# Performance work log

Hardware: AMD Instinct MI355X
Metric: run time of the kernel (lower is better)

The kernel has to match this reference:

```python
import jax, jax.numpy as jnp
import numpy as np

EPS = 1e-5
MAX_NORM = 1.0 - 1e-5  # clamp for atanh / ball projection


def mob_add(u, v):
    # Mobius addition on each d_ball (last dim), c=1
    uv = jnp.sum(u * v, axis=-1, keepdims=True)
    uu = jnp.sum(u * u, axis=-1, keepdims=True)
    vv = jnp.sum(v * v, axis=-1, keepdims=True)
    num = (1.0 + 2.0 * uv + vv) * u + (1.0 - uu) * v
    den = 1.0 + 2.0 * uv + uu * vv
    return num / jnp.maximum(den, EPS)


def log_map_zero(y):
    # log map at origin, per ball (last dim)
    n = jnp.linalg.norm(y, axis=-1, keepdims=True)
    n_c = jnp.clip(n, EPS, MAX_NORM)
    return jnp.arctanh(n_c) * y / n_c


def mob_mat_mul_d(W, x, d):
    # W: (n_in, d, n_out, d); x: (B, n_in, d) -> (B, n_out, d)
    # Mobius matvec on the flattened product-ball representation.
    B = x.shape[0]
    x_f = x.reshape(B, -1)                      # (B, n_in*d)
    W_f = W.reshape(x_f.shape[-1], -1)          # (n_in*d, n_out*d)
    Mx = x_f @ W_f                              # (B, n_out*d)
    x_n = jnp.clip(jnp.linalg.norm(x_f, axis=-1, keepdims=True), EPS, MAX_NORM)
    Mx_n = jnp.maximum(jnp.linalg.norm(Mx, axis=-1, keepdims=True), EPS)
    res = jnp.tanh(Mx_n / x_n * jnp.arctanh(x_n)) * (Mx / Mx_n)
    return res.reshape(B, -1, d)


def mob_pointwise_prod(x, u):
    # diagonal Mobius scaling of hyperbolic x by euclidean gate u, per ball
    ux = u * x
    x_n = jnp.clip(jnp.linalg.norm(x, axis=-1, keepdims=True), EPS, MAX_NORM)
    ux_n = jnp.maximum(jnp.linalg.norm(ux, axis=-1, keepdims=True), EPS)
    return jnp.tanh(ux_n / x_n * jnp.arctanh(x_n)) * (ux / ux_n)


def transition(W, h, U, x, b, d):
    Wh = mob_mat_mul_d(W, h, d)
    Ux = mob_mat_mul_d(U, x, d)
    return mob_add(mob_add(Wh, Ux), b)


def setup_inputs() -> dict:
    key = jax.random.key(0)
    ks = jax.random.split(key, 8)
    B, I, H, D = 16384, 256, 256, 4
    k = (1.0 / H) ** 0.5
    # scale points to lie strictly inside the Poincare ball
    hyp_x = 0.02 * jax.random.normal(ks[0], (B, I, D), dtype=jnp.float32)
    hidden = 0.02 * jax.random.normal(ks[1], (B, H, D), dtype=jnp.float32)
    mk = lambda kk, n_in: jax.random.uniform(kk, (n_in, D, H, D), minval=-k, maxval=k, dtype=jnp.float32)
    return dict(
        hyp_x=hyp_x, hidden=hidden,
        w_z=mk(ks[2], H), w_r=mk(ks[3], H), w_h=mk(ks[4], H),
        u_z=mk(ks[5], I), u_r=mk(ks[6], I), u_h=mk(ks[7], I),
        b_z=jnp.zeros((H, D), jnp.float32),
        b_r=jnp.zeros((H, D), jnp.float32),
        b_h=jnp.zeros((H, D), jnp.float32),
    )


def reference(hyp_x, hidden, w_z, w_r, w_h, u_z, u_r, u_h, b_z, b_r, b_h):
    d = hyp_x.shape[-1]
    z = jax.nn.sigmoid(log_map_zero(transition(w_z, hidden, u_z, hyp_x, b_z, d)))
    r = jax.nn.sigmoid(log_map_zero(transition(w_r, hidden, u_r, hyp_x, b_r, d)))
    r_point_h = mob_pointwise_prod(hidden, r)
    # NOTE: original code uses u_r here (not u_h) -- kept faithful
    h_tilde = transition(w_h, r_point_h, u_r, hyp_x, b_h, d)
    minus_h_oplus_htilde = mob_add(-hidden, h_tilde)
    new_h = mob_add(hidden, mob_pointwise_prod(minus_h_oplus_htilde, z))
    return new_h
```

## Files before the change

### kernel.cpp

```cpp
#include <hip/hip_runtime.h>
#include <stdint.h>

#define EPSF 1e-5f
#define MAXNF (1.0f - 1e-5f)

typedef __attribute__((ext_vector_type(8))) short short8;
typedef __attribute__((ext_vector_type(4))) float floatx4;

__device__ __forceinline__ unsigned short f2bf(float f){
  union { float f; uint32_t u; } v; v.f = f;
  return (unsigned short)((v.u + 0x7FFFu + ((v.u >> 16) & 1u)) >> 16);
}
__device__ __forceinline__ float bf_lo(uint32_t u){
  union { uint32_t u; float f; } v; v.u = u << 16; return v.f;
}
__device__ __forceinline__ float bf_hi(uint32_t u){
  union { uint32_t u; float f; } v; v.u = u & 0xffff0000u; return v.f;
}
__device__ __forceinline__ uint32_t cvtpk(float lo, float hi){
  uint32_t r; asm("v_cvt_pk_bf16_f32 %0, %1, %2" : "=v"(r) : "v"(lo), "v"(hi));
  return r;
}
__device__ __forceinline__ float fsqrt(float x){ return __builtin_amdgcn_sqrtf(x); }

__device__ __forceinline__ float4 ld_ball(const unsigned short* rowp, int b){
  const uint2 u = *(const uint2*)(rowp + 4*b);
  return make_float4(bf_lo(u.x), bf_hi(u.x), bf_lo(u.y), bf_hi(u.y));
}
__device__ __forceinline__ void st_ball(unsigned short* rowp, int b, float4 f){
  uint2 u; u.x = cvtpk(f.x, f.y); u.y = cvtpk(f.z, f.w);
  *(uint2*)(rowp + 4*b) = u;
}

__device__ __forceinline__ void gload16(const void* g, void* l){
  __builtin_amdgcn_global_load_lds(
      (__attribute__((address_space(1))) void*)(uintptr_t)g,
      (__attribute__((address_space(3))) void*)l, 16, 0, 0);
}

__device__ __forceinline__ float fatanh(float x){
  return 0.5f * __logf(__fdividef(1.f + x, 1.f - x));
}
__device__ __forceinline__ float ftanh_pos(float x){
  const float t = __expf(-2.f * x);
  return __fdividef(1.f - t, 1.f + t);
}
__device__ __forceinline__ float fsig(float x){
  return __fdividef(1.f, 1.f + __expf(-x));
}

__device__ __forceinline__ float wsum(float v){
  #pragma unroll
  for (int o = 32; o; o >>= 1) v += __shfl_xor(v, o);
  return v;
}

__device__ __forceinline__ float dot4(const float4 a, const float4 b){
  return a.x*b.x + a.y*b.y + a.z*b.z + a.w*b.w;
}
__device__ __forceinline__ float4 scal4(const float4 a, float s){
  return make_float4(a.x*s, a.y*s, a.z*s, a.w*s);
}
__device__ __forceinline__ float clipn(float n){ return fminf(fmaxf(n, EPSF), MAXNF); }

__device__ __forceinline__ float4 mob_add4(const float4 u, const float4 v){
  const float uv = dot4(u,v), uu = dot4(u,u), vv = dot4(v,v);
  const float cu = 1.f + 2.f*uv + vv, cv = 1.f - uu;
  const float inv = __fdividef(1.f, fmaxf(1.f + 2.f*uv + uu*vv, EPSF));
  return make_float4((cu*u.x + cv*v.x)*inv, (cu*u.y + cv*v.y)*inv,
                     (cu*u.z + cv*v.z)*inv, (cu*u.w + cv*v.w)*inv);
}
__device__ __forceinline__ float4 logmap_sig4(const float4 y){
  const float nc = clipn(fsqrt(dot4(y,y)));
  const float s = __fdividef(fatanh(nc), nc);
  return make_float4(fsig(s*y.x), fsig(s*y.y), fsig(s*y.z), fsig(s*y.w));
}
__device__ __forceinline__ float4 mob_pp4(const float4 x, const float4 u){
  const float4 ux = make_float4(u.x*x.x, u.y*x.y, u.z*x.z, u.w*x.w);
  const float xn = clipn(fsqrt(dot4(x,x)));
  const float uxn = fmaxf(fsqrt(dot4(ux,ux)), EPSF);
  const float s = __fdividef(ftanh_pos(__fdividef(uxn, xn) * fatanh(xn)), uxn);
  return scal4(ux, s);
}

__global__ void cast_norm_k(const float* __restrict__ X, unsigned short* __restrict__ Xbf,
                            float* __restrict__ nrm){
  const int lane = threadIdx.x & 63;
  const int row  = blockIdx.x*4 + (threadIdx.x >> 6);
  const float4* xr = (const float4*)(X + (size_t)row*1024);
  unsigned short* br_ = Xbf + (size_t)row*1024;
  float ss = 0.f;
  #pragma unroll
  for (int i = 0; i < 4; ++i){
    const int b = lane + 64*i;
    const float4 v = xr[b];
    st_ball(br_, b, v);
    ss += dot4(v, v);
  }
  ss = wsum(ss);
  if (lane == 0) nrm[row] = fsqrt(ss);
}

__global__ void wcast_k(const float* __restrict__ W, unsigned short* __restrict__ Wt){
  __shared__ float tile[32][33];
  const int tx = threadIdx.x, ty = threadIdx.y;
  const int k0 = blockIdx.x * 32, n0 = blockIdx.y * 32;
  #pragma unroll
  for (int i = 0; i < 4; ++i)
    tile[ty + i*8][tx] = W[(size_t)(k0 + ty + i*8) * 1024 + n0 + tx];
  __syncthreads();
  #pragma unroll
  for (int i = 0; i < 4; ++i)
    Wt[(size_t)(n0 + ty + i*8) * 1024 + k0 + tx] = f2bf(tile[tx][ty + i*8]);
}

#define NT 16

#define BARFENCE do { __builtin_amdgcn_s_barrier(); asm volatile("" ::: "memory"); } while(0)
#define LDA4(dst, MO, BUF) do { _Pragma("unroll") for (int m_=0;m_<4;++m_) \
  _Pragma("unroll") for (int k_=0;k_<2;++k_) \
    dst[m_][k_] = *(const short8*)(smem + (BUF)*32768 + abase + (MO+m_)*2048 + ((((k_<<2)+kg)^x7)<<4)); } while(0)
#define LDB2(dst, NO, BUF) do { _Pragma("unroll") for (int n_=0;n_<2;++n_) \
  _Pragma("unroll") for (int k_=0;k_<2;++k_) \
    dst[n_][k_] = *(const short8*)(smem + (BUF)*32768 + bbase + (NO+n_)*2048 + ((((k_<<2)+kg)^x7)<<4)); } while(0)
#define QUAD(AF, MO, BF, NO) do { _Pragma("unroll") for (int m_=0;m_<4;++m_) \
  _Pragma("unroll") for (int n_=0;n_<2;++n_) \
  _Pragma("unroll") for (int k_=0;k_<2;++k_) \
    acc[MO+m_][NO+n_] = __builtin_amdgcn_mfma_f32_16x16x32_bf16(AF[m_][k_], BF[n_][k_], acc[MO+m_][NO+n_], 0,0,0); } while(0)

__global__ __launch_bounds__(512, 2) void gemm8_k(const unsigned short* __restrict__ A,
                                                  const unsigned short* __restrict__ Bt,
                                                  unsigned short* __restrict__ C,
                                                  int lda, int ldc, int lnx){
  __shared__ unsigned char smem[131072];
  const int tid = threadIdx.x;
  const int lane = tid & 63, w = tid >> 6;
  const int wm = w >> 2, wn = w & 3;
  const int lr = lane & 15, kg = lane >> 4;
  const int x7 = lr & 7;

  const int wg  = blockIdx.x;
  const int xcd = wg & 7, q = wg >> 3;
  const int bx  = q & ((1 << lnx) - 1);
  const int by  = (xcd << 3) + (q >> lnx);
  const int row0 = by * 256, col0 = bx * 256;

  const int abase = (wm*128 + lr)*128;
  const int bbase = 65536 + (wn*64 + lr)*128;

  floatx4 acc[8][4] = {};

  auto stageH = [&](int regionByte, const unsigned short* src, int srow0, int ld, int kt){
    #pragma unroll
    for (int call = 0; call < 2; ++call){
      const int L  = (call << 9) + tid;
      const int rl = L >> 3;
      const int cc = (L & 7) ^ (rl & 7);
      gload16(src + (size_t)(srow0 + rl)*ld + kt*64 + cc*8,
              smem + regionByte + L*16);
    }
  };
  auto stageA = [&](int kt, int h){ stageH((kt&1)*32768 + h*16384, A, row0 + h*128, lda, kt); };
  auto stageB = [&](int kt, int h){ stageH(65536 + (kt&1)*32768 + h*16384, Bt, col0 + h*128, 1024, kt); };

  stageA(0,0); stageA(0,1); stageB(0,0); stageB(0,1);
  stageA(1,0); stageA(1,1); stageB(1,0); stageB(1,1);
  asm volatile("s_waitcnt vmcnt(8)" ::: "memory");
  BARFENCE;

  short8 aL[4][2], aH[4][2], bA[2][2], bB[2][2];
  LDA4(aL, 0, 0);
  LDB2(bA, 0, 0);

  for (int t = 0; t < NT; ++t){
    const int bufb = t & 1;
    LDB2(bB, 2, bufb);
    BARFENCE;
    __builtin_amdgcn_s_setprio(1); QUAD(aL, 0, bA, 0); __builtin_amdgcn_s_setprio(0);
    BARFENCE;
    LDA4(aH, 4, bufb);
    BARFENCE;
    __builtin_amdgcn_s_setprio(1); QUAD(aL, 0, bB, 2); __builtin_amdgcn_s_setprio(0);
    BARFENCE;
    if (t+2 < NT){
      stageB(t+2,0); stageB(t+2,1);
      asm volatile("s_waitcnt vmcnt(4)" ::: "memory");
    } else if (t+1 < NT){
      asm volatile("s_waitcnt vmcnt(0)" ::: "memory");
    }
    BARFENCE;
    __builtin_amdgcn_s_setprio(1); QUAD(aH, 4, bB, 2); __builtin_amdgcn_s_setprio(0);
    if (t+1 < NT) LDA4(aL, 0, bufb^1);
    BARFENCE;
    if (t+2 < NT){ stageA(t+2,0); stageA(t+2,1); }
    BARFENCE;
    __builtin_amdgcn_s_setprio(1); QUAD(aH, 4, bA, 0); __builtin_amdgcn_s_setprio(0);
    if (t+1 < NT) LDB2(bA, 0, bufb^1);
    BARFENCE;
  }

  const int crow = row0 + wm*128;
  const int ccol = col0 + wn*64 + lr;
  #pragma unroll
  for (int m = 0; m < 8; ++m){
    #pragma unroll
    for (int j = 0; j < 4; ++j){
      unsigned short* cp = C + (size_t)(crow + m*16 + kg*4 + j)*ldc + ccol;
      #pragma unroll
      for (int n = 0; n < 4; ++n) cp[n*16] = f2bf(acc[m][n][j]);
    }
  }
}

__global__ __launch_bounds__(256) __attribute__((amdgpu_waves_per_eu(4,4)))
void epi1_k(unsigned short* C1, unsigned short* C2, const unsigned short* hbf,
            const float* bz, const float* br,
            const float* h_nrm, const float* x_nrm, float* rph_nrm){
  const int lane = threadIdx.x & 63;
  const int row  = blockIdx.x*4 + (threadIdx.x >> 6);
  unsigned short* c1lo = C1 + (size_t)row*2048;
  unsigned short* c1hi = c1lo + 1024;
  unsigned short* c2lo = C2 + (size_t)row*2048;
  unsigned short* c2hi = c2lo + 1024;
  const unsigned short* hr = hbf + (size_t)row*1024;

  float4 mzh[4], mrh[4], mzx[4], mrx[4];
  float s0 = 0.f, s1 = 0.f, s2 = 0.f, s3 = 0.f;
  #pragma unroll
  for (int i = 0; i < 4; ++i){
    const int b = lane + 64*i;
    mzh[i] = ld_ball(c1lo, b); mrh[i] = ld_ball(c1hi, b);
    mzx[i] = ld_ball(c2lo, b); mrx[i] = ld_ball(c2hi, b);
    s0 += dot4(mzh[i], mzh[i]); s1 += dot4(mzx[i], mzx[i]);
    s2 += dot4(mrh[i], mrh[i]); s3 += dot4(mrx[i], mrx[i]);
  }
  s0 = wsum(s0); s1 = wsum(s1); s2 = wsum(s2); s3 = wsum(s3);

  const float nMzh = fmaxf(fsqrt(s0), EPSF);
  const float nMzx = fmaxf(fsqrt(s1), EPSF);
  const float nMrh = fmaxf(fsqrt(s2), EPSF);
  const float nMrx = fmaxf(fsqrt(s3), EPSF);
  const float hnc = clipn(h_nrm[row]), xnc = clipn(x_nrm[row]);
  const float atH = fatanh(hnc), atX = fatanh(xnc);
  const float swz = __fdividef(ftanh_pos(__fdividef(nMzh, hnc)*atH), nMzh);
  const float suz = __fdividef(ftanh_pos(__fdividef(nMzx, xnc)*atX), nMzx);
  const float swr = __fdividef(ftanh_pos(__fdividef(nMrh, hnc)*atH), nMrh);
  const float sur = __fdividef(ftanh_pos(__fdividef(nMrx, xnc)*atX), nMrx);

  float sr = 0.f;
  #pragma unroll
  for (int i = 0; i < 4; ++i){
    const int b = lane + 64*i;
    const float4 bz4 = ((const float4*)bz)[b];
    const float4 br4 = ((const float4*)br)[b];
    const float4 z4  = logmap_sig4(mob_add4(mob_add4(scal4(mzh[i],swz), scal4(mzx[i],suz)), bz4));
    const float4 UxR = scal4(mrx[i], sur);
    const float4 r4  = logmap_sig4(mob_add4(mob_add4(scal4(mrh[i],swr), UxR), br4));
    st_ball(c1lo, b, z4);
    st_ball(c1hi, b, UxR);
    const float4 h4  = ld_ball(hr, b);
    const float4 rph = mob_pp4(h4, r4);
    st_ball(c2lo, b, rph);
    sr += dot4(rph, rph);
  }
  sr = wsum(sr);
  if (lane == 0) rph_nrm[row] = fsqrt(sr);
}

__global__ __launch_bounds__(256) __attribute__((amdgpu_waves_per_eu(4,4)))
void epi2_k(const unsigned short* C1, const unsigned short* C2,
            const unsigned short* hbf, const float* bh,
            const float* rph_nrm, float* out){
  const int lane = threadIdx.x & 63;
  const int row  = blockIdx.x*4 + (threadIdx.x >> 6);
  const unsigned short* c1lo = C1 + (size_t)row*2048;
  const unsigned short* c1hi = c1lo + 1024;
  const unsigned short* c2hi = C2 + (size_t)row*2048 + 1024;
  const unsigned short* hr = hbf + (size_t)row*1024;
  float4* outr = (float4*)(out + (size_t)row*1024);

  float4 mh[4];
  float ss = 0.f;
  #pragma unroll
  for (int i = 0; i < 4; ++i){
    mh[i] = ld_ball(c2hi, lane + 64*i);
    ss += dot4(mh[i], mh[i]);
  }
  ss = wsum(ss);
  const float nMh = fmaxf(fsqrt(ss), EPSF);
  const float rnc = clipn(rph_nrm[row]);
  const float swh = __fdividef(ftanh_pos(__fdividef(nMh, rnc)*fatanh(rnc)), nMh);

  #pragma unroll
  for (int i = 0; i < 4; ++i){
    const int b = lane + 64*i;
    const float4 WhH = scal4(mh[i], swh);
    const float4 Ux4 = ld_ball(c1hi, b);
    const float4 bh4 = ((const float4*)bh)[b];
    const float4 ht  = mob_add4(mob_add4(WhH, Ux4), bh4);
    const float4 h4  = ld_ball(hr, b);
    const float4 nh4 = make_float4(-h4.x, -h4.y, -h4.z, -h4.w);
    const float4 m4  = mob_add4(nh4, ht);
    const float4 z4  = ld_ball(c1lo, b);
    const float4 p4  = mob_pp4(m4, z4);
    outr[b] = mob_add4(h4, p4);
  }
}

extern "C" void kernel_launch(void* const* d_in, const int* in_sizes, int n_in,
                              void* d_out, int out_size, void* d_ws, size_t ws_size,
                              hipStream_t stream) {
  (void)in_sizes; (void)n_in; (void)out_size; (void)ws_size;
  const float* hyp_x  = (const float*)d_in[0];
  const float* hidden = (const float*)d_in[1];
  const float* w_z = (const float*)d_in[2];
  const float* w_r = (const float*)d_in[3];
  const float* w_h = (const float*)d_in[4];
  const float* u_z = (const float*)d_in[5];
  const float* u_r = (const float*)d_in[6];
  const float* b_z = (const float*)d_in[8];
  const float* b_r = (const float*)d_in[9];
  const float* b_h = (const float*)d_in[10];
  float* out = (float*)d_out;

  const size_t NROW = 16384, MAT = NROW*1024;
  unsigned short* hbf = (unsigned short*)d_ws;
  unsigned short* xbf = hbf + MAT;
  unsigned short* C1  = xbf + MAT;
  unsigned short* wzr = C1 + 2*MAT;
  unsigned short* uzr = wzr + 2*1048576;
  unsigned short* wht = uzr + 2*1048576;
  float* h_n   = (float*)(wht + 1048576);
  float* x_n   = h_n + NROW;
  float* rph_n = x_n + NROW;
  unsigned short* C2 = (unsigned short*)d_out;

  cast_norm_k<<<dim3(4096), dim3(256), 0, stream>>>(hidden, hbf, h_n);
  cast_norm_k<<<dim3(4096), dim3(256), 0, stream>>>(hyp_x, xbf, x_n);

  dim3 wg(32, 32), wb(32, 8);
  wcast_k<<<wg, wb, 0, stream>>>(w_z, wzr);
  wcast_k<<<wg, wb, 0, stream>>>(w_r, wzr + 1048576);
  wcast_k<<<wg, wb, 0, stream>>>(u_z, uzr);
  wcast_k<<<wg, wb, 0, stream>>>(u_r, uzr + 1048576);
  wcast_k<<<wg, wb, 0, stream>>>(w_h, wht);

  gemm8_k<<<dim3(512), dim3(512), 0, stream>>>(hbf, wzr, C1, 1024, 2048, 3);
  gemm8_k<<<dim3(512), dim3(512), 0, stream>>>(xbf, uzr, C2, 1024, 2048, 3);

  epi1_k<<<dim3(4096), dim3(256), 0, stream>>>(C1, C2, hbf, b_z, b_r, h_n, x_n, rph_n);

  gemm8_k<<<dim3(256), dim3(512), 0, stream>>>(C2, wht, C2 + 1024, 2048, 2048, 2);

  epi2_k<<<dim3(4096), dim3(256), 0, stream>>>(C1, C2, hbf, b_h, rph_n, out);
}
```

Before: 324.0 us.

## Switch GEMM to 32x32x16 MFMA tiles and merge cast kernel launches

The GEMM inner loop now issues 32x32x16 bf16 MFMAs instead of 16x16x32 ones. The shared-memory fragment loads, accumulator layout and epilogue store mapping are rewritten to match the larger tile shape. This is meant to cut the number of MFMA and LDS instructions for the same work. Separately, the two activation cast kernels and the five weight cast/transpose kernels are each merged into a single launch to reduce launch overhead. The new swizzle and row mapping add risk of LDS bank conflicts or indexing errors.

```diff
diff --git a/kernel.cpp b/kernel.cpp
--- a/kernel.cpp
+++ b/kernel.cpp
@@ -6,6 +6,7 @@
 
 typedef __attribute__((ext_vector_type(8))) short short8;
 typedef __attribute__((ext_vector_type(4))) float floatx4;
+typedef __attribute__((ext_vector_type(16))) float floatx16;
 
 __device__ __forceinline__ unsigned short f2bf(float f){
   union { float f; uint32_t u; } v; v.f = f;
@@ -83,12 +84,17 @@
   return scal4(ux, s);
 }
 
-__global__ void cast_norm_k(const float* __restrict__ X, unsigned short* __restrict__ Xbf,
-                            float* __restrict__ nrm){
+__global__ void cast2_k(const float* __restrict__ H, const float* __restrict__ X,
+                        unsigned short* __restrict__ Hbf, unsigned short* __restrict__ Xbf,
+                        float* __restrict__ h_n, float* __restrict__ x_n){
+  int blk = blockIdx.x;
+  const float* src; unsigned short* dst; float* nrm;
+  if (blk < 4096){ src = H; dst = Hbf; nrm = h_n; }
+  else { src = X; dst = Xbf; nrm = x_n; blk -= 4096; }
   const int lane = threadIdx.x & 63;
-  const int row  = blockIdx.x*4 + (threadIdx.x >> 6);
-  const float4* xr = (const float4*)(X + (size_t)row*1024);
-  unsigned short* br_ = Xbf + (size_t)row*1024;
+  const int row  = blk*4 + (threadIdx.x >> 6);
+  const float4* xr = (const float4*)(src + (size_t)row*1024);
+  unsigned short* br_ = dst + (size_t)row*1024;
   float ss = 0.f;
   #pragma unroll
   for (int i = 0; i < 4; ++i){
@@ -101,7 +107,20 @@
   if (lane == 0) nrm[row] = fsqrt(ss);
 }
 
-__global__ void wcast_k(const float* __restrict__ W, unsigned short* __restrict__ Wt){
+__global__ void wcast5_k(const float* __restrict__ w_z, const float* __restrict__ w_r,
+                         const float* __restrict__ u_z, const float* __restrict__ u_r,
+                         const float* __restrict__ w_h,
+                         unsigned short* __restrict__ wzr, unsigned short* __restrict__ uzr,
+                         unsigned short* __restrict__ wht){
+  const int m = blockIdx.z;
+  const float* W; unsigned short* Wt;
+  switch (m){
+    case 0: W = w_z; Wt = wzr;           break;
+    case 1: W = w_r; Wt = wzr + 1048576; break;
+    case 2: W = u_z; Wt = uzr;           break;
+    case 3: W = u_r; Wt = uzr + 1048576; break;
+    default: W = w_h; Wt = wht;          break;
+  }
   __shared__ float tile[32][33];
   const int tx = threadIdx.x, ty = threadIdx.y;
   const int k0 = blockIdx.x * 32, n0 = blockIdx.y * 32;
@@ -117,16 +136,14 @@
 #define NT 16
 
 #define BARFENCE do { __builtin_amdgcn_s_barrier(); asm volatile("" ::: "memory"); } while(0)
-#define LDA4(dst, MO, BUF) do { _Pragma("unroll") for (int m_=0;m_<4;++m_) \
-  _Pragma("unroll") for (int k_=0;k_<2;++k_) \
-    dst[m_][k_] = *(const short8*)(smem + (BUF)*32768 + abase + (MO+m_)*2048 + ((((k_<<2)+kg)^x7)<<4)); } while(0)
-#define LDB2(dst, NO, BUF) do { _Pragma("unroll") for (int n_=0;n_<2;++n_) \
-  _Pragma("unroll") for (int k_=0;k_<2;++k_) \
-    dst[n_][k_] = *(const short8*)(smem + (BUF)*32768 + bbase + (NO+n_)*2048 + ((((k_<<2)+kg)^x7)<<4)); } while(0)
-#define QUAD(AF, MO, BF, NO) do { _Pragma("unroll") for (int m_=0;m_<4;++m_) \
-  _Pragma("unroll") for (int n_=0;n_<2;++n_) \
-  _Pragma("unroll") for (int k_=0;k_<2;++k_) \
-    acc[MO+m_][NO+n_] = __builtin_amdgcn_mfma_f32_16x16x32_bf16(AF[m_][k_], BF[n_][k_], acc[MO+m_][NO+n_], 0,0,0); } while(0)
+#define LDA8(dst, MT0, BUF) do { _Pragma("unroll") for (int mt_=0;mt_<2;++mt_) \
+  _Pragma("unroll") for (int ks_=0;ks_<4;++ks_) \
+    dst[mt_][ks_] = *(const short8*)(smem + (BUF)*32768 + abase + (MT0+mt_)*4096 + ((((ks_<<1)+hi)^x7)<<4)); } while(0)
+#define LDB4(dst, NT0, BUF) do { _Pragma("unroll") for (int ks_=0;ks_<4;++ks_) \
+    dst[ks_] = *(const short8*)(smem + (BUF)*32768 + bbase + (NT0)*4096 + ((((ks_<<1)+hi)^x7)<<4)); } while(0)
+#define OCT(AF, MO, BF, NO) do { _Pragma("unroll") for (int mt_=0;mt_<2;++mt_) \
+  _Pragma("unroll") for (int ks_=0;ks_<4;++ks_) \
+    acc[MO+mt_][NO] = __builtin_amdgcn_mfma_f32_32x32x16_bf16(AF[mt_][ks_], BF[ks_], acc[MO+mt_][NO], 0,0,0); } while(0)
 
 __global__ __launch_bounds__(512, 2) void gemm8_k(const unsigned short* __restrict__ A,
                                                   const unsigned short* __restrict__ Bt,
@@ -136,8 +153,8 @@
   const int tid = threadIdx.x;
   const int lane = tid & 63, w = tid >> 6;
   const int wm = w >> 2, wn = w & 3;
-  const int lr = lane & 15, kg = lane >> 4;
-  const int x7 = lr & 7;
+  const int l31 = lane & 31, hi = lane >> 5;
+  const int x7 = lane & 7;
 
   const int wg  = blockIdx.x;
   const int xcd = wg & 7, q = wg >> 3;
@@ -145,10 +162,10 @@
   const int by  = (xcd << 3) + (q >> lnx);
   const int row0 = by * 256, col0 = bx * 256;
 
-  const int abase = (wm*128 + lr)*128;
-  const int bbase = 65536 + (wn*64 + lr)*128;
-
-  floatx4 acc[8][4] = {};
+  const int abase = (wm*128 + l31)*128;
+  const int bbase = 65536 + (wn*64 + l31)*128;
+
+  floatx16 acc[4][2] = {};
 
   auto stageH = [&](int regionByte, const unsigned short* src, int srow0, int ld, int kt){
     #pragma unroll
@@ -168,19 +185,19 @@
   asm volatile("s_waitcnt vmcnt(8)" ::: "memory");
   BARFENCE;
 
-  short8 aL[4][2], aH[4][2], bA[2][2], bB[2][2];
-  LDA4(aL, 0, 0);
-  LDB2(bA, 0, 0);
+  short8 aLo[2][4], aHi[2][4], bA[4], bB[4];
+  LDA8(aLo, 0, 0);
+  LDB4(bA, 0, 0);
 
   for (int t = 0; t < NT; ++t){
     const int bufb = t & 1;
-    LDB2(bB, 2, bufb);
-    BARFENCE;
-    __builtin_amdgcn_s_setprio(1); QUAD(aL, 0, bA, 0); __builtin_amdgcn_s_setprio(0);
-    BARFENCE;
-    LDA4(aH, 4, bufb);
-    BARFENCE;
-    __builtin_amdgcn_s_setprio(1); QUAD(aL, 0, bB, 2); __builtin_amdgcn_s_setprio(0);
+    LDB4(bB, 1, bufb);
+    BARFENCE;
+    __builtin_amdgcn_s_setprio(1); OCT(aLo, 0, bA, 0); __builtin_amdgcn_s_setprio(0);
+    BARFENCE;
+    LDA8(aHi, 2, bufb);
+    BARFENCE;
+    __builtin_amdgcn_s_setprio(1); OCT(aLo, 0, bB, 1); __builtin_amdgcn_s_setprio(0);
     BARFENCE;
     if (t+2 < NT){
       stageB(t+2,0); stageB(t+2,1);
@@ -189,25 +206,26 @@
       asm volatile("s_waitcnt vmcnt(0)" ::: "memory");
     }
     BARFENCE;
-    __builtin_amdgcn_s_setprio(1); QUAD(aH, 4, bB, 2); __builtin_amdgcn_s_setprio(0);
-    if (t+1 < NT) LDA4(aL, 0, bufb^1);
+    __builtin_amdgcn_s_setprio(1); OCT(aHi, 2, bB, 1); __builtin_amdgcn_s_setprio(0);
+    if (t+1 < NT) LDA8(aLo, 0, bufb^1);
     BARFENCE;
     if (t+2 < NT){ stageA(t+2,0); stageA(t+2,1); }
     BARFENCE;
-    __builtin_amdgcn_s_setprio(1); QUAD(aH, 4, bA, 0); __builtin_amdgcn_s_setprio(0);
-    if (t+1 < NT) LDB2(bA, 0, bufb^1);
+    __builtin_amdgcn_s_setprio(1); OCT(aHi, 2, bA, 0); __builtin_amdgcn_s_setprio(0);
+    if (t+1 < NT) LDB4(bA, 0, bufb^1);
     BARFENCE;
   }
 
   const int crow = row0 + wm*128;
-  const int ccol = col0 + wn*64 + lr;
-  #pragma unroll
-  for (int m = 0; m < 8; ++m){
+  const int ccol = col0 + wn*64 + l31;
+  #pragma unroll
+  for (int mt = 0; mt < 4; ++mt){
     #pragma unroll
-    for (int j = 0; j < 4; ++j){
-      unsigned short* cp = C + (size_t)(crow + m*16 + kg*4 + j)*ldc + ccol;
-      #pragma unroll
-      for (int n = 0; n < 4; ++n) cp[n*16] = f2bf(acc[m][n][j]);
+    for (int r = 0; r < 16; ++r){
+      const int row = crow + mt*32 + (r&3) + 8*(r>>2) + 4*hi;
+      unsigned short* cp = C + (size_t)row*ldc + ccol;
+      cp[0]  = f2bf(acc[mt][0][r]);
+      cp[32] = f2bf(acc[mt][1][r]);
     }
   }
 }
@@ -335,15 +353,9 @@
   float* rph_n = x_n + NROW;
   unsigned short* C2 = (unsigned short*)d_out;
 
-  cast_norm_k<<<dim3(4096), dim3(256), 0, stream>>>(hidden, hbf, h_n);
-  cast_norm_k<<<dim3(4096), dim3(256), 0, stream>>>(hyp_x, xbf, x_n);
-
-  dim3 wg(32, 32), wb(32, 8);
-  wcast_k<<<wg, wb, 0, stream>>>(w_z, wzr);
-  wcast_k<<<wg, wb, 0, stream>>>(w_r, wzr + 1048576);
-  wcast_k<<<wg, wb, 0, stream>>>(u_z, uzr);
-  wcast_k<<<wg, wb, 0, stream>>>(u_r, uzr + 1048576);
-  wcast_k<<<wg, wb, 0, stream>>>(w_h, wht);
+  cast2_k<<<dim3(8192), dim3(256), 0, stream>>>(hidden, hyp_x, hbf, xbf, h_n, x_n);
+  wcast5_k<<<dim3(32,32,5), dim3(32,8), 0, stream>>>(w_z, w_r, u_z, u_r, w_h,
+                                                     wzr, uzr, wht);
 
   gemm8_k<<<dim3(512), dim3(512), 0, stream>>>(hbf, wzr, C1, 1024, 2048, 3);
   gemm8_k<<<dim3(512), dim3(512), 0, stream>>>(xbf, uzr, C2, 1024, 2048, 3);
```

Result: no change. 325.8 us (+0.5%).
